# Kernel tuning notes

Hardware: AMD Instinct MI355X
Metric: run time of the kernel (lower is better)

The kernel has to match this reference:

```python
import jax, jax.numpy as jnp
import numpy as np


def gcn_layer(x, src, dst, W, b, n_dst):
    # DGL GraphConv, norm='both': D_src^{-1/2} pre-norm, sum aggregate, D_dst^{-1/2} post-norm, + bias
    n_src = x.shape[0]
    e_ones = jnp.ones(src.shape[0], dtype=x.dtype)
    deg_out = jnp.clip(jax.ops.segment_sum(e_ones, src, num_segments=n_src), 1.0)
    deg_in = jnp.clip(jax.ops.segment_sum(e_ones, dst, num_segments=n_dst), 1.0)
    h = (x * jax.lax.rsqrt(deg_out)[:, None]) @ W          # [n_src, out]
    agg = jax.ops.segment_sum(h[src], dst, num_segments=n_dst)  # [n_dst, out]
    return jax.nn.relu(agg * jax.lax.rsqrt(deg_in)[:, None] + b)


def setup_inputs() -> dict:
    key = jax.random.key(0)
    ks = jax.random.split(key, 8)
    N_SRC0, N_DST0, N_DST1 = 400000, 40000, 4000
    E0, E1 = 400000, 40000
    D_IN, D_HID, D_OUT = 256, 256, 256
    x = jax.random.normal(ks[0], (N_SRC0, D_IN), dtype=jnp.float32)
    src0 = jax.random.randint(ks[1], (E0,), 0, N_SRC0)
    dst0 = jax.random.randint(ks[2], (E0,), 0, N_DST0)
    src1 = jax.random.randint(ks[3], (E1,), 0, N_DST0)
    dst1 = jax.random.randint(ks[4], (E1,), 0, N_DST1)
    W0 = jax.random.normal(ks[5], (D_IN, D_HID), dtype=jnp.float32) * (1.0 / np.sqrt(D_IN))
    W1 = jax.random.normal(ks[6], (D_HID, D_OUT), dtype=jnp.float32) * (1.0 / np.sqrt(D_HID))
    b0 = jnp.zeros((D_HID,), dtype=jnp.float32)
    b1 = jnp.zeros((D_OUT,), dtype=jnp.float32)
    return {"x": x, "src0": src0, "dst0": dst0, "src1": src1, "dst1": dst1,
            "W0": W0, "b0": b0, "W1": W1, "b1": b1,
            "n_dst0": N_DST0, "n_dst1": N_DST1}


def reference(x, src0, dst0, src1, dst1, W0, b0, W1, b1, n_dst0, n_dst1):
    h = gcn_layer(x, src0, dst0, W0, b0, n_dst0)   # [n_dst0, hidden]
    out = gcn_layer(h, src1, dst1, W1, b1, n_dst1)  # [n_dst1, out]
    return out
```

## Files before the change

kernel.cpp:

```cpp
#include <hip/hip_runtime.h>
#include <hip/hip_bf16.h>
#include <cstddef>
#include <cstdint>


#define D 256
#define N_DST0_CONST 40000

typedef __attribute__((ext_vector_type(8))) short s16x8;
typedef __attribute__((ext_vector_type(4))) short s16x4;
typedef __attribute__((ext_vector_type(4))) float f32x4;

__device__ inline short f2bf(float f) {
    __hip_bfloat16 h = __float2bfloat16(f);
    return *reinterpret_cast<short*>(&h);
}

__global__ void zero_i(int* __restrict__ p, int n) {
    int i = blockIdx.x * blockDim.x + threadIdx.x;
    int stride = gridDim.x * blockDim.x;
    for (; i < n; i += stride) p[i] = 0;
}

__global__ void count_deg_both(const int* __restrict__ src0, const int* __restrict__ dst0, int E0,
                               const int* __restrict__ src1, const int* __restrict__ dst1, int E1,
                               int* __restrict__ cs0, int* __restrict__ cd0,
                               int* __restrict__ cs1, int* __restrict__ cd1) {
    int e = blockIdx.x * blockDim.x + threadIdx.x;
    if (e < E0) {
        atomicAdd(&cs0[src0[e]], 1);
        atomicAdd(&cd0[dst0[e]], 1);
    } else if (e < E0 + E1) {
        int i = e - E0;
        atomicAdd(&cs1[src1[i]], 1);
        atomicAdd(&cd1[dst1[i]], 1);
    }
}

__global__ __launch_bounds__(1024) void ex_scan_both(
    const int* __restrict__ cnt0, int* __restrict__ ptr0, int n0,
    const int* __restrict__ cnt1, int* __restrict__ ptr1, int n1) {
    const int* cnt = (blockIdx.x == 0) ? cnt0 : cnt1;
    int* ptr = (blockIdx.x == 0) ? ptr0 : ptr1;
    int n = (blockIdx.x == 0) ? n0 : n1;

    __shared__ int wsum[16];
    const int tid = threadIdx.x;
    const int chunk = (n + 1023) / 1024;
    const int begin = min(tid * chunk, n);
    const int end = min(begin + chunk, n);
    int local = 0;
    for (int i = begin; i < end; ++i) local += cnt[i];
    const int lane = tid & 63;
    const int wid = tid >> 6;
    int v = local;
    for (int off = 1; off < 64; off <<= 1) {
        int u = __shfl_up(v, off, 64);
        if (lane >= off) v += u;
    }
    if (lane == 63) wsum[wid] = v;
    __syncthreads();
    if (wid == 0 && lane < 16) {
        int w = wsum[lane];
        for (int off = 1; off < 16; off <<= 1) {
            int u = __shfl_up(w, off, 16);
            if (lane >= off) w += u;
        }
        wsum[lane] = w;
    }
    __syncthreads();
    int base = (wid > 0 ? wsum[wid - 1] : 0) + (v - local);
    int run = base;
    for (int i = begin; i < end; ++i) { ptr[i] = run; run += cnt[i]; }
}

__global__ void fill_csr_both(const int* __restrict__ src0, const int* __restrict__ dst0, int E0,
                              const int* __restrict__ src1, const int* __restrict__ dst1, int E1,
                              int* __restrict__ ptr0, int* __restrict__ es0,
                              int* __restrict__ ptr1, int* __restrict__ es1) {
    int e = blockIdx.x * blockDim.x + threadIdx.x;
    if (e < E0) {
        int pos = atomicAdd(&ptr0[dst0[e]], 1);
        es0[pos] = src0[e];
    } else if (e < E0 + E1) {
        int i = e - E0;
        int pos = atomicAdd(&ptr1[dst1[i]], 1);
        es1[pos] = src1[i];
    }
}

__global__ __launch_bounds__(256) void gather_agg_bf16(
    const float* __restrict__ X, const int* __restrict__ edge_src,
    const int* __restrict__ ptr, const int* __restrict__ cnt_src,
    short* __restrict__ agg, int nrows) {
    int d = blockIdx.x * 4 + threadIdx.y;
    if (d >= nrows) return;
    int beg = (d == 0) ? 0 : ptr[d - 1];
    int end = ptr[d];
    int deg = end - beg;
    int lane = threadIdx.x;

    int s_l = 0;
    float rn_l = 0.f;
    if (lane < deg) {
        s_l = edge_src[beg + lane];
        rn_l = rsqrtf(fmaxf((float)cnt_src[s_l], 1.0f));
    }

    float4 acc = make_float4(0.f, 0.f, 0.f, 0.f);
    int nb = min(deg, 64);
    int j = 0;
    for (; j + 4 <= nb; j += 4) {
        int s0 = __shfl(s_l, j + 0), s1 = __shfl(s_l, j + 1);
        int s2 = __shfl(s_l, j + 2), s3 = __shfl(s_l, j + 3);
        float r0 = __shfl(rn_l, j + 0), r1 = __shfl(rn_l, j + 1);
        float r2 = __shfl(rn_l, j + 2), r3 = __shfl(rn_l, j + 3);
        float4 v0 = *(const float4*)(X + (size_t)s0 * D + lane * 4);
        float4 v1 = *(const float4*)(X + (size_t)s1 * D + lane * 4);
        float4 v2 = *(const float4*)(X + (size_t)s2 * D + lane * 4);
        float4 v3 = *(const float4*)(X + (size_t)s3 * D + lane * 4);
        acc.x += v0.x * r0 + v1.x * r1 + v2.x * r2 + v3.x * r3;
        acc.y += v0.y * r0 + v1.y * r1 + v2.y * r2 + v3.y * r3;
        acc.z += v0.z * r0 + v1.z * r1 + v2.z * r2 + v3.z * r3;
        acc.w += v0.w * r0 + v1.w * r1 + v2.w * r2 + v3.w * r3;
    }
    for (; j < nb; ++j) {
        int s = __shfl(s_l, j);
        float r = __shfl(rn_l, j);
        float4 v = *(const float4*)(X + (size_t)s * D + lane * 4);
        acc.x += v.x * r; acc.y += v.y * r; acc.z += v.z * r; acc.w += v.w * r;
    }
    for (int jj = beg + 64; jj < end; ++jj) {
        int s = edge_src[jj];
        float r = rsqrtf(fmaxf((float)cnt_src[s], 1.0f));
        float4 v = *(const float4*)(X + (size_t)s * D + lane * 4);
        acc.x += v.x * r; acc.y += v.y * r; acc.z += v.z * r; acc.w += v.w * r;
    }

    s16x4 o;
    o.x = f2bf(acc.x); o.y = f2bf(acc.y); o.z = f2bf(acc.z); o.w = f2bf(acc.w);
    *(s16x4*)(agg + (size_t)d * D + lane * 4) = o;
}

__global__ __launch_bounds__(256) void transpose_cast_w_both(
    const float* __restrict__ Wa, short* __restrict__ BTa,
    const float* __restrict__ Wb, short* __restrict__ BTb) {
    const float* W = (blockIdx.z == 0) ? Wa : Wb;
    short* BT = (blockIdx.z == 0) ? BTa : BTb;
    __shared__ float t[16][17];
    int k0 = blockIdx.x * 16, n0 = blockIdx.y * 16;
    t[threadIdx.y][threadIdx.x] = W[(size_t)(k0 + threadIdx.y) * D + n0 + threadIdx.x];
    __syncthreads();
    BT[(size_t)(n0 + threadIdx.y) * D + k0 + threadIdx.x] = f2bf(t[threadIdx.x][threadIdx.y]);
}

#define LDK 40

__global__ __launch_bounds__(256) void gemm_bf16_mfma(
    const short* __restrict__ A, const short* __restrict__ BT,
    const int* __restrict__ cnt_dst, const float* __restrict__ bias,
    float* __restrict__ out, int M) {
    __shared__ short As[128][LDK];
    __shared__ short Bs[128][LDK];

    const int tid = threadIdx.x;
    const int m0 = blockIdx.x * 128;
    const int n0 = blockIdx.y * 128;
    const int wave = tid >> 6;
    const int lane = tid & 63;
    const int l15 = lane & 15;
    const int quad = lane >> 4;
    const int mo = (wave & 1) * 64;
    const int no = (wave >> 1) * 64;

    f32x4 acc[4][4] = {};

    for (int k0 = 0; k0 < D; k0 += 32) {
#pragma unroll
        for (int i = 0; i < 2; ++i) {
            int idx = tid + i * 256;
            int row = idx >> 2;
            int kg = (idx & 3) * 8;
            int gm = m0 + row;
            s16x8 av = {};
            if (gm < M) av = *(const s16x8*)(A + (size_t)gm * D + k0 + kg);
            *(s16x8*)&As[row][kg] = av;
            s16x8 bv = *(const s16x8*)(BT + (size_t)(n0 + row) * D + k0 + kg);
            *(s16x8*)&Bs[row][kg] = bv;
        }
        __syncthreads();

        s16x8 af[4], bf[4];
#pragma unroll
        for (int mt = 0; mt < 4; ++mt)
            af[mt] = *(const s16x8*)&As[mo + mt * 16 + l15][quad * 8];
#pragma unroll
        for (int nt = 0; nt < 4; ++nt)
            bf[nt] = *(const s16x8*)&Bs[no + nt * 16 + l15][quad * 8];
#pragma unroll
        for (int mt = 0; mt < 4; ++mt)
#pragma unroll
            for (int nt = 0; nt < 4; ++nt)
                acc[mt][nt] = __builtin_amdgcn_mfma_f32_16x16x32_bf16(
                    af[mt], bf[nt], acc[mt][nt], 0, 0, 0);
        __syncthreads();
    }

#pragma unroll
    for (int mt = 0; mt < 4; ++mt) {
#pragma unroll
        for (int r = 0; r < 4; ++r) {
            int gm = m0 + mo + mt * 16 + quad * 4 + r;
            if (gm >= M) continue;
            float sc = rsqrtf(fmaxf((float)cnt_dst[gm], 1.0f));
#pragma unroll
            for (int nt = 0; nt < 4; ++nt) {
                int gn = n0 + no + nt * 16 + l15;
                float v = fmaxf(acc[mt][nt][r] * sc + bias[gn], 0.f);
                out[(size_t)gm * D + gn] = v;
            }
        }
    }
}


extern "C" void kernel_launch(void* const* d_in, const int* in_sizes, int n_in,
                              void* d_out, int out_size, void* d_ws, size_t ws_size,
                              hipStream_t stream) {
    const float* x    = (const float*)d_in[0];
    const int*   src0 = (const int*)d_in[1];
    const int*   dst0 = (const int*)d_in[2];
    const int*   src1 = (const int*)d_in[3];
    const int*   dst1 = (const int*)d_in[4];
    const float* W0   = (const float*)d_in[5];
    const float* b0   = (const float*)d_in[6];
    const float* W1   = (const float*)d_in[7];
    const float* b1   = (const float*)d_in[8];

    const int n_src0 = in_sizes[0] / D;
    const int E0     = in_sizes[1];
    const int E1     = in_sizes[3];
    const int n_dst0 = N_DST0_CONST;
    const int n_dst1 = out_size / D;

    char* base = (char*)d_ws;
    size_t off = 0;
    auto alloc = [&](size_t bytes) { void* p = base + off; off = (off + bytes + 63) & ~(size_t)63; return p; };

    int* icnt = (int*)alloc((size_t)(n_src0 + 2 * n_dst0 + n_dst1) * 4);
    int* icnt_src0 = icnt;
    int* icnt_dst0 = icnt + n_src0;
    int* icnt_src1 = icnt + n_src0 + n_dst0;
    int* icnt_dst1 = icnt + n_src0 + 2 * n_dst0;
    const int cnt_total = n_src0 + 2 * n_dst0 + n_dst1;

    int* ptr0      = (int*)alloc((size_t)n_dst0 * 4);
    int* ptr1      = (int*)alloc((size_t)n_dst1 * 4);
    int* edge_src0 = (int*)alloc((size_t)E0 * 4);
    int* edge_src1 = (int*)alloc((size_t)E1 * 4);

    float* h0    = (float*)alloc((size_t)n_dst0 * D * 4);
    short* aggb0 = (short*)alloc((size_t)n_dst0 * D * 2);
    short* aggb1 = (short*)alloc((size_t)n_dst1 * D * 2);
    short* BT0   = (short*)alloc((size_t)D * D * 2);
    short* BT1   = (short*)alloc((size_t)D * D * 2);

    float* out = (float*)d_out;

    zero_i<<<512, 256, 0, stream>>>(icnt, cnt_total);

    count_deg_both<<<(E0 + E1 + 255) / 256, 256, 0, stream>>>(
        src0, dst0, E0, src1, dst1, E1, icnt_src0, icnt_dst0, icnt_src1, icnt_dst1);

    ex_scan_both<<<2, 1024, 0, stream>>>(icnt_dst0, ptr0, n_dst0, icnt_dst1, ptr1, n_dst1);

    fill_csr_both<<<(E0 + E1 + 255) / 256, 256, 0, stream>>>(
        src0, dst0, E0, src1, dst1, E1, ptr0, edge_src0, ptr1, edge_src1);

    {
        dim3 g(D / 16, D / 16, 2), b(16, 16);
        transpose_cast_w_both<<<g, b, 0, stream>>>(W0, BT0, W1, BT1);
    }

    {
        dim3 blk(64, 4);
        gather_agg_bf16<<<(n_dst0 + 3) / 4, blk, 0, stream>>>(x, edge_src0, ptr0, icnt_src0, aggb0, n_dst0);
        dim3 grid((n_dst0 + 127) / 128, D / 128);
        gemm_bf16_mfma<<<grid, 256, 0, stream>>>(aggb0, BT0, icnt_dst0, b0, h0, n_dst0);
    }

    {
        dim3 blk(64, 4);
        gather_agg_bf16<<<(n_dst1 + 3) / 4, blk, 0, stream>>>(h0, edge_src1, ptr1, icnt_src1, aggb1, n_dst1);
        dim3 grid((n_dst1 + 127) / 128, D / 128);
        gemm_bf16_mfma<<<grid, 256, 0, stream>>>(aggb1, BT1, icnt_dst1, b1, out, n_dst1);
    }
}
```

Measured before the change: 697.9 us.

## Skip layer-0 rows unused by layer 1 and fold weight transpose into degree count

```diff
diff --git a/kernel.cpp b/kernel.cpp
--- a/kernel.cpp
+++ b/kernel.cpp
@@ -22,19 +22,38 @@
     for (; i < n; i += stride) p[i] = 0;
 }
 
-__global__ void count_deg_both(const int* __restrict__ src0, const int* __restrict__ dst0, int E0,
-                               const int* __restrict__ src1, const int* __restrict__ dst1, int E1,
-                               int* __restrict__ cs0, int* __restrict__ cd0,
-                               int* __restrict__ cs1, int* __restrict__ cd1) {
-    int e = blockIdx.x * blockDim.x + threadIdx.x;
-    if (e < E0) {
-        atomicAdd(&cs0[src0[e]], 1);
-        atomicAdd(&cd0[dst0[e]], 1);
-    } else if (e < E0 + E1) {
-        int i = e - E0;
-        atomicAdd(&cs1[src1[i]], 1);
-        atomicAdd(&cd1[dst1[i]], 1);
-    }
+__global__ __launch_bounds__(256) void count_deg_tr_both(
+    const int* __restrict__ src0, const int* __restrict__ dst0, int E0,
+    const int* __restrict__ src1, const int* __restrict__ dst1, int E1,
+    int* __restrict__ cs0, int* __restrict__ cd0,
+    int* __restrict__ cs1, int* __restrict__ cd1,
+    int nEdgeBlocks,
+    const float* __restrict__ Wa, short* __restrict__ BTa,
+    const float* __restrict__ Wb, short* __restrict__ BTb) {
+    int b = blockIdx.x;
+    if (b < nEdgeBlocks) {
+        int e = b * 256 + threadIdx.x;
+        if (e < E0) {
+            atomicAdd(&cs0[src0[e]], 1);
+            atomicAdd(&cd0[dst0[e]], 1);
+        } else if (e < E0 + E1) {
+            int i = e - E0;
+            atomicAdd(&cs1[src1[i]], 1);
+            atomicAdd(&cd1[dst1[i]], 1);
+        }
+        return;
+    }
+    int t = b - nEdgeBlocks;
+    const float* W = (t < 256) ? Wa : Wb;
+    short* BT = (t < 256) ? BTa : BTb;
+    t &= 255;
+    int k0 = (t & 15) * 16;
+    int n0 = (t >> 4) * 16;
+    __shared__ float tile[16][17];
+    int tx = threadIdx.x & 15, ty = threadIdx.x >> 4;
+    tile[ty][tx] = W[(size_t)(k0 + ty) * D + n0 + tx];
+    __syncthreads();
+    BT[(size_t)(n0 + ty) * D + k0 + tx] = f2bf(tile[tx][ty]);
 }
 
 __global__ __launch_bounds__(1024) void ex_scan_both(
@@ -92,9 +111,11 @@
 __global__ __launch_bounds__(256) void gather_agg_bf16(
     const float* __restrict__ X, const int* __restrict__ edge_src,
     const int* __restrict__ ptr, const int* __restrict__ cnt_src,
+    const int* __restrict__ needed,
     short* __restrict__ agg, int nrows) {
     int d = blockIdx.x * 4 + threadIdx.y;
     if (d >= nrows) return;
+    if (needed && needed[d] == 0) return;
     int beg = (d == 0) ? 0 : ptr[d - 1];
     int end = ptr[d];
     int deg = end - beg;
@@ -142,18 +163,6 @@
     *(s16x4*)(agg + (size_t)d * D + lane * 4) = o;
 }
 
-__global__ __launch_bounds__(256) void transpose_cast_w_both(
-    const float* __restrict__ Wa, short* __restrict__ BTa,
-    const float* __restrict__ Wb, short* __restrict__ BTb) {
-    const float* W = (blockIdx.z == 0) ? Wa : Wb;
-    short* BT = (blockIdx.z == 0) ? BTa : BTb;
-    __shared__ float t[16][17];
-    int k0 = blockIdx.x * 16, n0 = blockIdx.y * 16;
-    t[threadIdx.y][threadIdx.x] = W[(size_t)(k0 + threadIdx.y) * D + n0 + threadIdx.x];
-    __syncthreads();
-    BT[(size_t)(n0 + threadIdx.y) * D + k0 + threadIdx.x] = f2bf(t[threadIdx.x][threadIdx.y]);
-}
-
 #define LDK 40
 
 __global__ __launch_bounds__(256) void gemm_bf16_mfma(
@@ -269,8 +278,11 @@
 
     zero_i<<<512, 256, 0, stream>>>(icnt, cnt_total);
 
-    count_deg_both<<<(E0 + E1 + 255) / 256, 256, 0, stream>>>(
-        src0, dst0, E0, src1, dst1, E1, icnt_src0, icnt_dst0, icnt_src1, icnt_dst1);
+    const int nEdgeBlocks = (E0 + E1 + 255) / 256;
+    count_deg_tr_both<<<nEdgeBlocks + 512, 256, 0, stream>>>(
+        src0, dst0, E0, src1, dst1, E1,
+        icnt_src0, icnt_dst0, icnt_src1, icnt_dst1,
+        nEdgeBlocks, W0, BT0, W1, BT1);
 
     ex_scan_both<<<2, 1024, 0, stream>>>(icnt_dst0, ptr0, n_dst0, icnt_dst1, ptr1, n_dst1);
 
@@ -278,20 +290,17 @@
         src0, dst0, E0, src1, dst1, E1, ptr0, edge_src0, ptr1, edge_src1);
 
     {
-        dim3 g(D / 16, D / 16, 2), b(16, 16);
-        transpose_cast_w_both<<<g, b, 0, stream>>>(W0, BT0, W1, BT1);
+        dim3 blk(64, 4);
+        gather_agg_bf16<<<(n_dst0 + 3) / 4, blk, 0, stream>>>(
+            x, edge_src0, ptr0, icnt_src0, icnt_src1, aggb0, n_dst0);
+        dim3 grid((n_dst0 + 127) / 128, D / 128);
+        gemm_bf16_mfma<<<grid, 256, 0, stream>>>(aggb0, BT0, icnt_dst0, b0, h0, n_dst0);
     }
 
     {
         dim3 blk(64, 4);
-        gather_agg_bf16<<<(n_dst0 + 3) / 4, blk, 0, stream>>>(x, edge_src0, ptr0, icnt_src0, aggb0, n_dst0);
-        dim3 grid((n_dst0 + 127) / 128, D / 128);
-        gemm_bf16_mfma<<<grid, 256, 0, stream>>>(aggb0, BT0, icnt_dst0, b0, h0, n_dst0);
-    }
-
-    {
-        dim3 blk(64, 4);
-        gather_agg_bf16<<<(n_dst1 + 3) / 4, blk, 0, stream>>>(h0, edge_src1, ptr1, icnt_src1, aggb1, n_dst1);
+        gather_agg_bf16<<<(n_dst1 + 3) / 4, blk, 0, stream>>>(
+            h0, edge_src1, ptr1, icnt_src1, nullptr, aggb1, n_dst1);
         dim3 grid((n_dst1 + 127) / 128, D / 128);
         gemm_bf16_mfma<<<grid, 256, 0, stream>>>(aggb1, BT1, icnt_dst1, b1, out, n_dst1);
     }
```

New measurement: 672.6 us. -3.6%, faster.
